# Kernel tuning notes

Measured on AMD Instinct MI355X. Metric: run time of the kernel, lower is better.

The kernel has to match this reference:

```python
import jax, jax.numpy as jnp
import numpy as np

B, S, D = 2, 2048, 1024
N, H = 16, 64  # n_heads, d_head
INIT_STD = 0.02
IGNORE = -100000.0


def setup_inputs() -> dict:
    key = jax.random.key(0)
    ks = jax.random.split(key, 6)
    return {
        "normalized_resid_pre": jax.random.normal(ks[0], (B, S, D), dtype=jnp.float32),
        "W_Q": jax.random.normal(ks[1], (N, D, H), dtype=jnp.float32) * INIT_STD,
        "W_K": jax.random.normal(ks[2], (N, D, H), dtype=jnp.float32) * INIT_STD,
        "W_V": jax.random.normal(ks[3], (N, D, H), dtype=jnp.float32) * INIT_STD,
        "W_O": jax.random.normal(ks[4], (N, H, D), dtype=jnp.float32) * INIT_STD,
        "b_Q": jnp.zeros((N, H), dtype=jnp.float32),
        "b_K": jnp.zeros((N, H), dtype=jnp.float32),
        "b_V": jnp.zeros((N, H), dtype=jnp.float32),
        "b_O": jnp.zeros((D,), dtype=jnp.float32),
    }


def reference(normalized_resid_pre, W_Q, W_K, W_V, W_O, b_Q, b_K, b_V, b_O):
    x = normalized_resid_pre
    q = jnp.einsum('ndh,bpd->bpnh', W_Q, x) + b_Q
    k = jnp.einsum('ndh,bpd->bpnh', W_K, x) + b_K
    v = jnp.einsum('ndh,bpd->bpnh', W_V, x) + b_V
    scores = jnp.einsum('bpnh,bsnh->bnps', q, k) / jnp.sqrt(jnp.float32(H))
    # causal mask: key_pos > query_pos -> IGNORE
    seq = scores.shape[-1]
    mask = jnp.triu(jnp.ones((seq, seq), dtype=bool), k=1)
    scores = jnp.where(mask, jnp.float32(IGNORE), scores)
    attn = jax.nn.softmax(scores, axis=-1)
    z = jnp.einsum('bnps,bsnh->bpnh', attn, v)
    # per-head out-proj then sum over heads
    out = jnp.einsum('bpnh,nhd->bpd', z, W_O) + b_O
    return out
```

## Files before the change

### kernel.cpp

```cpp
#include <hip/hip_runtime.h>
#include <math.h>

#define S_ 2048
#define D_ 1024
#define N_ 16
#define H_ 64
#define M_ 4096

typedef float f4 __attribute__((ext_vector_type(4)));
typedef float f16v __attribute__((ext_vector_type(16)));
typedef short s8v __attribute__((ext_vector_type(8)));
typedef short s4v __attribute__((ext_vector_type(4)));
typedef unsigned short u16;

#define MFMA32(a, b, c) __builtin_amdgcn_mfma_f32_32x32x16_bf16((a), (b), (c), 0, 0, 0)

__device__ __forceinline__ u16 f2bf(float x) {
    unsigned int u = __float_as_uint(x);
    u += 0x7fffu + ((u >> 16) & 1u);
    return (u16)(u >> 16);
}
union FragU { unsigned int u[4]; s4v h[2]; s8v v; };

__device__ __forceinline__ s8v ld8(const u16* p) {
    FragU f;
    f.h[0] = *(const s4v*)(p);
    f.h[1] = *(const s4v*)(p + 4);
    return f.v;
}
__device__ __forceinline__ void st8(u16* p, s8v x) {
    FragU f; f.v = x;
    *(s4v*)(p)     = f.h[0];
    *(s4v*)(p + 4) = f.h[1];
}

__global__ __launch_bounds__(256) void cvt_x(const float* __restrict__ x,
                                             u16* __restrict__ xb)
{
    int i = (blockIdx.x * 256 + threadIdx.x) * 8;
    f4 a = *(const f4*)(x + i);
    f4 b = *(const f4*)(x + i + 4);
    unsigned long long p0 =
        (unsigned long long)f2bf(a[0]) | ((unsigned long long)f2bf(a[1]) << 16) |
        ((unsigned long long)f2bf(a[2]) << 32) | ((unsigned long long)f2bf(a[3]) << 48);
    unsigned long long p1 =
        (unsigned long long)f2bf(b[0]) | ((unsigned long long)f2bf(b[1]) << 16) |
        ((unsigned long long)f2bf(b[2]) << 32) | ((unsigned long long)f2bf(b[3]) << 48);
    *(unsigned long long*)(xb + i)     = p0;
    *(unsigned long long*)(xb + i + 4) = p1;
}

__global__ __launch_bounds__(256) void transW_kernel(
    const float* __restrict__ Wq, const float* __restrict__ Wk, const float* __restrict__ Wv,
    u16* __restrict__ Wc)
{
    const int which = blockIdx.z, n = blockIdx.y, dt = blockIdx.x;
    const float* W = which == 0 ? Wq : (which == 1 ? Wk : Wv);
    __shared__ float t[64][65];
    const int tid = threadIdx.x;
    #pragma unroll
    for (int it = 0; it < 4; ++it) {
        int c = tid + it * 256;
        int d = c >> 4, h4 = c & 15;
        f4 v = *(const f4*)(W + ((size_t)n * 1024 + dt * 64 + d) * 64 + h4 * 4);
        #pragma unroll
        for (int j = 0; j < 4; ++j) t[h4 * 4 + j][d] = v[j];
    }
    __syncthreads();
    #pragma unroll
    for (int it = 0; it < 4; ++it) {
        int c = tid + it * 256;
        int h = c >> 4, d4 = c & 15;
        size_t o = (size_t)(which * 1024 + n * 64 + h) * 1024 + dt * 64 + d4 * 4;
        *(unsigned long long*)(Wc + o) =
            (unsigned long long)f2bf(t[h][d4 * 4 + 0]) |
            ((unsigned long long)f2bf(t[h][d4 * 4 + 1]) << 16) |
            ((unsigned long long)f2bf(t[h][d4 * 4 + 2]) << 32) |
            ((unsigned long long)f2bf(t[h][d4 * 4 + 3]) << 48);
    }
}

__global__ __launch_bounds__(256) void transWo_kernel(
    const float* __restrict__ Wo, u16* __restrict__ WoT)
{
    const int rt = blockIdx.y, ct = blockIdx.x;
    __shared__ float t[64][65];
    const int tid = threadIdx.x;
    #pragma unroll
    for (int it = 0; it < 4; ++it) {
        int c = tid + it * 256;
        int r = c >> 4, c4 = c & 15;
        f4 v = *(const f4*)(Wo + (size_t)(rt * 64 + r) * 1024 + ct * 64 + c4 * 4);
        #pragma unroll
        for (int j = 0; j < 4; ++j) t[c4 * 4 + j][r] = v[j];
    }
    __syncthreads();
    #pragma unroll
    for (int it = 0; it < 4; ++it) {
        int c = tid + it * 256;
        int d = c >> 4, r4 = c & 15;
        size_t o = (size_t)(ct * 64 + d) * 1024 + rt * 64 + r4 * 4;
        *(unsigned long long*)(WoT + o) =
            (unsigned long long)f2bf(t[d][r4 * 4 + 0]) |
            ((unsigned long long)f2bf(t[d][r4 * 4 + 1]) << 16) |
            ((unsigned long long)f2bf(t[d][r4 * 4 + 2]) << 32) |
            ((unsigned long long)f2bf(t[d][r4 * 4 + 3]) << 48);
    }
}

__global__ void bcat_kernel(const float* bq, const float* bk, const float* bv, float* bc)
{
    int i = blockIdx.x * 256 + threadIdx.x;
    bc[i] = i < 1024 ? bq[i] : (i < 2048 ? bk[i - 1024] : bv[i - 2048]);
}

template<int MODE>
__global__ __launch_bounds__(256) void gemm_bf16(
    const u16* __restrict__ A, const u16* __restrict__ B,
    const float* __restrict__ bias,
    u16* __restrict__ outq, u16* __restrict__ outk, u16* __restrict__ outvT,
    float* __restrict__ outf)
{
    __shared__ u16 sm[17408];
    u16* Ash = sm;
    u16* Bsh = sm + 8704;

    const int tid = threadIdx.x;
    const int lane = tid & 63, w = tid >> 6;
    const int wm = w & 1, wn = w >> 1;
    const int l31 = lane & 31, hi = lane >> 5;
    const int m0 = blockIdx.x * 128, n0 = blockIdx.y * 128;

    f16v acc[2][2];
    #pragma unroll
    for (int a = 0; a < 2; ++a)
        #pragma unroll
        for (int b = 0; b < 2; ++b)
            #pragma unroll
            for (int r = 0; r < 16; ++r) acc[a][b][r] = 0.f;

    for (int kt = 0; kt < 16; ++kt) {
        __syncthreads();
        #pragma unroll
        for (int t = 0; t < 4; ++t) {
            int c = tid + t * 256;
            int row = c >> 3, c8 = c & 7;
            int idx = row * 68 + c8 * 8;
            s8v av = *(const s8v*)(A + (size_t)(m0 + row) * 1024 + kt * 64 + c8 * 8);
            s8v bv = *(const s8v*)(B + (size_t)(n0 + row) * 1024 + kt * 64 + c8 * 8);
            st8(&Ash[idx], av);
            st8(&Bsh[idx], bv);
        }
        __syncthreads();
        #pragma unroll
        for (int ks = 0; ks < 4; ++ks) {
            const int off = (2 * ks + hi) * 8;
            s8v af[2], bf[2];
            #pragma unroll
            for (int mb = 0; mb < 2; ++mb)
                af[mb] = ld8(&Ash[(64 * wm + 32 * mb + l31) * 68 + off]);
            #pragma unroll
            for (int nb = 0; nb < 2; ++nb)
                bf[nb] = ld8(&Bsh[(64 * wn + 32 * nb + l31) * 68 + off]);
            #pragma unroll
            for (int mb = 0; mb < 2; ++mb)
                #pragma unroll
                for (int nb = 0; nb < 2; ++nb)
                    acc[mb][nb] = MFMA32(af[mb], bf[nb], acc[mb][nb]);
        }
    }

    __syncthreads();

    if constexpr (MODE == 0) {
        u16* Zw = sm + w * 4096;
        const int which = n0 >> 10;
        #pragma unroll
        for (int nb = 0; nb < 2; ++nb) {
            int nhl = 32 * nb + l31;
            float bv = bias[n0 + 64 * wn + nhl];
            #pragma unroll
            for (int mb = 0; mb < 2; ++mb)
                #pragma unroll
                for (int r = 0; r < 16; ++r) {
                    int ml = 32 * mb + (r & 3) + 8 * (r >> 2) + 4 * hi;
                    u16 hv = f2bf(acc[mb][nb][r] + bv);
                    int idx = (which == 2)
                        ? nhl * 64 + (ml ^ ((nhl & 7) << 3))
                        : ml * 64 + (nhl ^ ((ml & 7) << 3));
                    Zw[idx] = hv;
                }
        }
        __syncthreads();
        const int gmb = m0 + 64 * wm;
        const int gnb = n0 + 64 * wn;
        #pragma unroll
        for (int it = 0; it < 8; ++it) {
            int c = lane + it * 64;
            int row = c >> 3, c8 = c & 7;
            int idx = row * 64 + 8 * (c8 ^ (row & 7));
            s8v val = *(const s8v*)&Zw[idx];
            if (which == 0)
                *(s8v*)(outq + (size_t)(gmb + row) * 1024 + gnb + c8 * 8) = val;
            else if (which == 1)
                *(s8v*)(outk + (size_t)(gmb + row) * 1024 + (gnb - 1024) + c8 * 8) = val;
            else
                *(s8v*)(outvT + (size_t)(gnb - 2048 + row) * 4096 + gmb + c8 * 8) = val;
        }
    } else {
        #pragma unroll
        for (int nb = 0; nb < 2; ++nb) {
            int gcol = n0 + 64 * wn + 32 * nb + l31;
            float bv = bias[gcol];
            #pragma unroll
            for (int mb = 0; mb < 2; ++mb)
                #pragma unroll
                for (int r = 0; r < 16; ++r) {
                    int gm = m0 + 64 * wm + 32 * mb + (r & 3) + 8 * (r >> 2) + 4 * hi;
                    outf[(size_t)gm * 1024 + gcol] = acc[mb][nb][r] + bv;
                }
        }
    }
}

#define SCALE_LOG2 (0.125f * 1.44269504088896340736f)

__global__ __launch_bounds__(256) void attn_mfma(
    const u16* __restrict__ qp, const u16* __restrict__ kp,
    const u16* __restrict__ vTp, u16* __restrict__ zp)
{
    __shared__ u16 sm[8704];
    u16* Ksh = sm;
    u16* Vsh = sm + 4352;

    const int tid = threadIdx.x;
    const int lane = tid & 63, w = tid >> 6;
    const int l31 = lane & 31, hi = lane >> 5;
    const int qt = (int)gridDim.x - 1 - (int)blockIdx.x;
    const int n = blockIdx.y, b = blockIdx.z;
    const int q0 = qt * 128;
    const int qrow = q0 + 32 * w + l31;
    const size_t mrow = (size_t)b * 2048 + qrow;

    s8v qf[4];
    #pragma unroll
    for (int c = 0; c < 4; ++c)
        qf[c] = *(const s8v*)(qp + mrow * 1024 + n * 64 + c * 16 + hi * 8);

    f16v acc[2];
    #pragma unroll
    for (int mb = 0; mb < 2; ++mb)
        #pragma unroll
        for (int r = 0; r < 16; ++r) acc[mb][r] = 0.f;
    float mrun = -1e30f, lrun = 0.f;
    const int nkt = 2 * qt + 2;
    const int wqmax = q0 + 32 * w + 31;

    for (int kt = 0; kt < nkt; ++kt) {
        __syncthreads();
        #pragma unroll
        for (int t2 = 0; t2 < 2; ++t2) {
            int c = tid + t2 * 256;
            int row = c >> 3, c8 = c & 7;
            int idx = row * 68 + c8 * 8;
            s8v kv = *(const s8v*)(kp + ((size_t)b * 2048 + kt * 64 + row) * 1024 + n * 64 + c8 * 8);
            s8v vv = *(const s8v*)(vTp + ((size_t)n * 64 + row) * 4096 + b * 2048 + kt * 64 + c8 * 8);
            st8(&Ksh[idx], kv);
            st8(&Vsh[idx], vv);
        }
        __syncthreads();
        if (64 * kt > wqmax) continue;

        f16v sf[2];
        #pragma unroll
        for (int t = 0; t < 2; ++t) {
            #pragma unroll
            for (int r = 0; r < 16; ++r) sf[t][r] = 0.f;
            int row = 32 * t + l31;
            #pragma unroll
            for (int c = 0; c < 4; ++c) {
                s8v kf = ld8(&Ksh[row * 68 + (2 * c + hi) * 8]);
                sf[t] = MFMA32(kf, qf[c], sf[t]);
            }
        }

        float mloc = -1e30f;
        #pragma unroll
        for (int t = 0; t < 2; ++t)
            #pragma unroll
            for (int r = 0; r < 16; ++r) {
                float sc = sf[t][r] * SCALE_LOG2;
                int sg = kt * 64 + 32 * t + (r & 3) + 8 * (r >> 2) + 4 * hi;
                if (sg > qrow) sc = -1e30f;
                sf[t][r] = sc;
                mloc = fmaxf(mloc, sc);
            }
        mloc = fmaxf(mloc, __shfl_xor(mloc, 32, 64));
        float mnew = fmaxf(mrun, mloc);
        float alpha = exp2f(mrun - mnew);
        float ls = 0.f;
        #pragma unroll
        for (int t = 0; t < 2; ++t)
            #pragma unroll
            for (int r = 0; r < 16; ++r) {
                float pv = exp2f(sf[t][r] - mnew);
                sf[t][r] = pv;
                ls += pv;
            }
        ls += __shfl_xor(ls, 32, 64);
        lrun = lrun * alpha + ls;
        mrun = mnew;
        #pragma unroll
        for (int mb = 0; mb < 2; ++mb)
            #pragma unroll
            for (int r = 0; r < 16; ++r) acc[mb][r] *= alpha;

        s8v pf[4];
        #pragma unroll
        for (int c = 0; c < 4; ++c) {
            const int i0 = 2 * c, i1 = 2 * c + 1;
            const int t0 = i0 >> 2, u0 = i0 & 3;
            const int t1 = i1 >> 2, u1 = i1 & 3;
            unsigned int f00 = (unsigned int)f2bf(sf[t0][4 * u0 + 0]) |
                               ((unsigned int)f2bf(sf[t0][4 * u0 + 1]) << 16);
            unsigned int f01 = (unsigned int)f2bf(sf[t0][4 * u0 + 2]) |
                               ((unsigned int)f2bf(sf[t0][4 * u0 + 3]) << 16);
            unsigned int f10 = (unsigned int)f2bf(sf[t1][4 * u1 + 0]) |
                               ((unsigned int)f2bf(sf[t1][4 * u1 + 1]) << 16);
            unsigned int f11 = (unsigned int)f2bf(sf[t1][4 * u1 + 2]) |
                               ((unsigned int)f2bf(sf[t1][4 * u1 + 3]) << 16);
            unsigned int s0 = hi ? f00 : f10, s1 = hi ? f01 : f11;
            unsigned int r0 = __shfl_xor(s0, 32, 64);
            unsigned int r1 = __shfl_xor(s1, 32, 64);
            FragU f;
            f.u[0] = hi ? r0 : f00;  f.u[1] = hi ? r1 : f01;
            f.u[2] = hi ? f10 : r0;  f.u[3] = hi ? f11 : r1;
            pf[c] = f.v;
        }

        #pragma unroll
        for (int mb = 0; mb < 2; ++mb) {
            int row = 32 * mb + l31;
            #pragma unroll
            for (int c = 0; c < 4; ++c) {
                s8v vf = ld8(&Vsh[row * 68 + (2 * c + hi) * 8]);
                acc[mb] = MFMA32(vf, pf[c], acc[mb]);
            }
        }
    }

    __syncthreads();
    float linv = 1.0f / lrun;
    u16* Z = sm + w * 2048;
    #pragma unroll
    for (int mb = 0; mb < 2; ++mb)
        #pragma unroll
        for (int r = 0; r < 16; ++r) {
            int hcol = 32 * mb + (r & 3) + 8 * (r >> 2) + 4 * hi;
            int idx = l31 * 64 + (hcol ^ ((l31 & 7) << 3));
            Z[idx] = f2bf(acc[mb][r] * linv);
        }
    __syncthreads();
    #pragma unroll
    for (int it = 0; it < 4; ++it) {
        int c = lane + it * 64;
        int row = c >> 3, c8 = c & 7;
        int idx = row * 64 + 8 * (c8 ^ (row & 7));
        *(s8v*)(zp + ((size_t)b * 2048 + q0 + 32 * w + row) * 1024 + n * 64 + c8 * 8) =
            *(const s8v*)&Z[idx];
    }
}

extern "C" void kernel_launch(void* const* d_in, const int* in_sizes, int n_in,
                              void* d_out, int out_size, void* d_ws, size_t ws_size,
                              hipStream_t stream) {
    const float* x  = (const float*)d_in[0];
    const float* Wq = (const float*)d_in[1];
    const float* Wk = (const float*)d_in[2];
    const float* Wv = (const float*)d_in[3];
    const float* Wo = (const float*)d_in[4];
    const float* bq = (const float*)d_in[5];
    const float* bk = (const float*)d_in[6];
    const float* bv = (const float*)d_in[7];
    const float* bO = (const float*)d_in[8];
    float* out = (float*)d_out;

    char* p = (char*)d_ws;
    size_t o = 0;
    auto alloc = [&](size_t bytes) { char* r = p + o; o += bytes; return r; };
    const size_t MB8 = (size_t)M_ * D_ * 2;
    u16* xb   = (u16*)alloc(MB8);
    u16* Wc   = (u16*)alloc((size_t)3072 * 1024 * 2);
    u16* WoT  = (u16*)alloc((size_t)1024 * 1024 * 2);
    float* bc = (float*)alloc(65536);
    u16* qb   = (u16*)alloc(MB8);
    u16* kb   = (u16*)alloc(MB8);
    u16* vTb  = (u16*)alloc(MB8);
    if (ws_size < o) return;
    u16* zb = xb;

    cvt_x<<<2048, 256, 0, stream>>>(x, xb);
    transW_kernel<<<dim3(16, 16, 3), 256, 0, stream>>>(Wq, Wk, Wv, Wc);
    transWo_kernel<<<dim3(16, 16), 256, 0, stream>>>(Wo, WoT);
    bcat_kernel<<<12, 256, 0, stream>>>(bq, bk, bv, bc);
    gemm_bf16<0><<<dim3(32, 24), 256, 0, stream>>>(
        xb, Wc, bc, qb, kb, vTb, nullptr);
    attn_mfma<<<dim3(16, 16, 2), 256, 0, stream>>>(qb, kb, vTb, zb);
    gemm_bf16<1><<<dim3(32, 8), 256, 0, stream>>>(
        zb, WoT, bO, nullptr, nullptr, nullptr, out);
}
```

Baseline: 255.7 us.

## Double-buffer attention K/V via direct global-to-LDS loads with swizzled layout

Replaces the register-staged LDS fills in both the projection GEMM and the attention kernel with global_load_lds 16-byte direct copies, using an XOR-swizzled unpadded LDS layout. Attention now double-buffers K/V tiles so the next tile's load overlaps the current tile's compute. It also folds the softmax scale into Q at projection time, uses packed bf16 conversion instructions, skips the causal mask on fully visible tiles, and defers the running-max rescale when the max grows by at most 8. These aim to cut load latency, bank conflicts and VALU work, but they double attention LDS usage and rely on careful barrier placement for the async loads.

```diff
diff --git a/kernel.cpp b/kernel.cpp
--- a/kernel.cpp
+++ b/kernel.cpp
@@ -3,36 +3,33 @@
 
 #define S_ 2048
 #define D_ 1024
-#define N_ 16
-#define H_ 64
 #define M_ 4096
 
 typedef float f4 __attribute__((ext_vector_type(4)));
 typedef float f16v __attribute__((ext_vector_type(16)));
 typedef short s8v __attribute__((ext_vector_type(8)));
-typedef short s4v __attribute__((ext_vector_type(4)));
 typedef unsigned short u16;
 
-#define MFMA32(a, b, c) __builtin_amdgcn_mfma_f32_32x32x16_bf16((a), (b), (c), 0, 0, 0)
+#define MFMA32(a,b,c) __builtin_amdgcn_mfma_f32_32x32x16_bf16((a),(b),(c),0,0,0)
+#define QSCALE 0.1803368801111204f
+#define NINF  -1e30f
 
 __device__ __forceinline__ u16 f2bf(float x) {
     unsigned int u = __float_as_uint(x);
     u += 0x7fffu + ((u >> 16) & 1u);
     return (u16)(u >> 16);
 }
-union FragU { unsigned int u[4]; s4v h[2]; s8v v; };
-
-__device__ __forceinline__ s8v ld8(const u16* p) {
-    FragU f;
-    f.h[0] = *(const s4v*)(p);
-    f.h[1] = *(const s4v*)(p + 4);
-    return f.v;
-}
-__device__ __forceinline__ void st8(u16* p, s8v x) {
-    FragU f; f.v = x;
-    *(s4v*)(p)     = f.h[0];
-    *(s4v*)(p + 4) = f.h[1];
-}
+__device__ __forceinline__ unsigned int cvtpk(float lo, float hi) {
+    unsigned int r;
+    asm("v_cvt_pk_bf16_f32 %0, %1, %2" : "=v"(r) : "v"(lo), "v"(hi));
+    return r;
+}
+__device__ __forceinline__ void gload16(const void* g, void* l) {
+    __builtin_amdgcn_global_load_lds(
+        (const __attribute__((address_space(1))) unsigned int*)g,
+        (__attribute__((address_space(3))) unsigned int*)l, 16, 0, 0);
+}
+union FragU { unsigned int u[4]; s8v v; };
 
 __global__ __launch_bounds__(256) void cvt_x(const float* __restrict__ x,
                                              u16* __restrict__ xb)
@@ -121,15 +118,18 @@
     u16* __restrict__ outq, u16* __restrict__ outk, u16* __restrict__ outvT,
     float* __restrict__ outf)
 {
-    __shared__ u16 sm[17408];
+    __shared__ u16 sm[16384];
     u16* Ash = sm;
-    u16* Bsh = sm + 8704;
+    u16* Bsh = sm + 8192;
 
     const int tid = threadIdx.x;
     const int lane = tid & 63, w = tid >> 6;
     const int wm = w & 1, wn = w >> 1;
     const int l31 = lane & 31, hi = lane >> 5;
     const int m0 = blockIdx.x * 128, n0 = blockIdx.y * 128;
+    const int srow = lane >> 3;
+    const int sc8 = (lane & 7) ^ srow;
+    const int rx = l31 & 7;
 
     f16v acc[2][2];
     #pragma unroll
@@ -142,26 +142,24 @@
     for (int kt = 0; kt < 16; ++kt) {
         __syncthreads();
         #pragma unroll
-        for (int t = 0; t < 4; ++t) {
-            int c = tid + t * 256;
-            int row = c >> 3, c8 = c & 7;
-            int idx = row * 68 + c8 * 8;
-            s8v av = *(const s8v*)(A + (size_t)(m0 + row) * 1024 + kt * 64 + c8 * 8);
-            s8v bv = *(const s8v*)(B + (size_t)(n0 + row) * 1024 + kt * 64 + c8 * 8);
-            st8(&Ash[idx], av);
-            st8(&Bsh[idx], bv);
+        for (int i = 0; i < 4; ++i) {
+            const int rb = (i * 4 + w) * 8;
+            const int row = rb + srow;
+            gload16(A + (size_t)(m0 + row) * 1024 + kt * 64 + sc8 * 8, Ash + rb * 64);
+            gload16(B + (size_t)(n0 + row) * 1024 + kt * 64 + sc8 * 8, Bsh + rb * 64);
         }
         __syncthreads();
         #pragma unroll
         for (int ks = 0; ks < 4; ++ks) {
-            const int off = (2 * ks + hi) * 8;
             s8v af[2], bf[2];
             #pragma unroll
             for (int mb = 0; mb < 2; ++mb)
-                af[mb] = ld8(&Ash[(64 * wm + 32 * mb + l31) * 68 + off]);
+                af[mb] = *(const s8v*)&Ash[(64 * wm + 32 * mb + l31) * 64 +
+                                           ((2 * ks + hi) ^ rx) * 8];
             #pragma unroll
             for (int nb = 0; nb < 2; ++nb)
-                bf[nb] = ld8(&Bsh[(64 * wn + 32 * nb + l31) * 68 + off]);
+                bf[nb] = *(const s8v*)&Bsh[(64 * wn + 32 * nb + l31) * 64 +
+                                           ((2 * ks + hi) ^ rx) * 8];
             #pragma unroll
             for (int mb = 0; mb < 2; ++mb)
                 #pragma unroll
@@ -184,7 +182,9 @@
                 #pragma unroll
                 for (int r = 0; r < 16; ++r) {
                     int ml = 32 * mb + (r & 3) + 8 * (r >> 2) + 4 * hi;
-                    u16 hv = f2bf(acc[mb][nb][r] + bv);
+                    float vv = acc[mb][nb][r] + bv;
+                    if (which == 0) vv *= QSCALE;
+                    u16 hv = f2bf(vv);
                     int idx = (which == 2)
                         ? nhl * 64 + (ml ^ ((nhl & 7) << 3))
                         : ml * 64 + (nhl ^ ((ml & 7) << 3));
@@ -223,16 +223,11 @@
     }
 }
 
-#define SCALE_LOG2 (0.125f * 1.44269504088896340736f)
-
 __global__ __launch_bounds__(256) void attn_mfma(
     const u16* __restrict__ qp, const u16* __restrict__ kp,
     const u16* __restrict__ vTp, u16* __restrict__ zp)
 {
-    __shared__ u16 sm[8704];
-    u16* Ksh = sm;
-    u16* Vsh = sm + 4352;
-
+    __shared__ u16 sm[16384];
     const int tid = threadIdx.x;
     const int lane = tid & 63, w = tid >> 6;
     const int l31 = lane & 31, hi = lane >> 5;
@@ -240,7 +235,11 @@
     const int n = blockIdx.y, b = blockIdx.z;
     const int q0 = qt * 128;
     const int qrow = q0 + 32 * w + l31;
+    const int wqmin = q0 + 32 * w, wqmax = wqmin + 31;
     const size_t mrow = (size_t)b * 2048 + qrow;
+    const int srow = lane >> 3;
+    const int sc8 = (lane & 7) ^ srow;
+    const int rx = l31 & 7;
 
     s8v qf[4];
     #pragma unroll
@@ -252,101 +251,130 @@
     for (int mb = 0; mb < 2; ++mb)
         #pragma unroll
         for (int r = 0; r < 16; ++r) acc[mb][r] = 0.f;
-    float mrun = -1e30f, lrun = 0.f;
+    float mrun = NINF, lrun = 0.f;
     const int nkt = 2 * qt + 2;
-    const int wqmax = q0 + 32 * w + 31;
-
+
+    auto STAGE = [&](int kt, int bufi) {
+        u16* Kd = sm + bufi * 8192;
+        u16* Vd = Kd + 4096;
+        #pragma unroll
+        for (int i = 0; i < 2; ++i) {
+            const int rb = (i * 4 + w) * 8;
+            const int row = rb + srow;
+            gload16(kp + ((size_t)b * 2048 + kt * 64 + row) * 1024 + n * 64 + sc8 * 8,
+                    Kd + rb * 64);
+            gload16(vTp + ((size_t)n * 64 + row) * 4096 + b * 2048 + kt * 64 + sc8 * 8,
+                    Vd + rb * 64);
+        }
+    };
+
+    STAGE(0, 0);
+    int cur = 0;
     for (int kt = 0; kt < nkt; ++kt) {
         __syncthreads();
-        #pragma unroll
-        for (int t2 = 0; t2 < 2; ++t2) {
-            int c = tid + t2 * 256;
-            int row = c >> 3, c8 = c & 7;
-            int idx = row * 68 + c8 * 8;
-            s8v kv = *(const s8v*)(kp + ((size_t)b * 2048 + kt * 64 + row) * 1024 + n * 64 + c8 * 8);
-            s8v vv = *(const s8v*)(vTp + ((size_t)n * 64 + row) * 4096 + b * 2048 + kt * 64 + c8 * 8);
-            st8(&Ksh[idx], kv);
-            st8(&Vsh[idx], vv);
-        }
-        __syncthreads();
-        if (64 * kt > wqmax) continue;
-
-        f16v sf[2];
-        #pragma unroll
-        for (int t = 0; t < 2; ++t) {
-            #pragma unroll
-            for (int r = 0; r < 16; ++r) sf[t][r] = 0.f;
-            int row = 32 * t + l31;
+        if (kt + 1 < nkt) STAGE(kt + 1, cur ^ 1);
+        if (64 * kt <= wqmax) {
+            const u16* Kd = sm + cur * 8192;
+            const u16* Vd = Kd + 4096;
+
+            f16v sf[2];
+            #pragma unroll
+            for (int t = 0; t < 2; ++t) {
+                #pragma unroll
+                for (int r = 0; r < 16; ++r) sf[t][r] = 0.f;
+                const int row = 32 * t + l31;
+                #pragma unroll
+                for (int c = 0; c < 4; ++c) {
+                    s8v kf = *(const s8v*)&Kd[row * 64 + ((2 * c + hi) ^ rx) * 8];
+                    sf[t] = MFMA32(kf, qf[c], sf[t]);
+                }
+            }
+
+            if (64 * kt + 63 > wqmin) {
+                #pragma unroll
+                for (int t = 0; t < 2; ++t)
+                    #pragma unroll
+                    for (int r = 0; r < 16; ++r) {
+                        const int sg = kt * 64 + 32 * t + (r & 3) + 8 * (r >> 2) + 4 * hi;
+                        if (sg > qrow) sf[t][r] = NINF;
+                    }
+            }
+
+            float ma = NINF, mb2 = NINF, mc = NINF, md = NINF;
+            #pragma unroll
+            for (int t = 0; t < 2; ++t)
+                #pragma unroll
+                for (int r = 0; r < 16; r += 4) {
+                    ma  = fmaxf(ma,  sf[t][r]);
+                    mb2 = fmaxf(mb2, sf[t][r + 1]);
+                    mc  = fmaxf(mc,  sf[t][r + 2]);
+                    md  = fmaxf(md,  sf[t][r + 3]);
+                }
+            float mloc = fmaxf(fmaxf(ma, mb2), fmaxf(mc, md));
+            mloc = fmaxf(mloc, __shfl_xor(mloc, 32, 64));
+
+            float mbase;
+            bool defer = (mloc - mrun <= 8.0f);
+            if (__all(defer)) {
+                mbase = mrun;
+            } else {
+                float mnew = fmaxf(mrun, mloc);
+                float alpha = exp2f(mrun - mnew);
+                lrun *= alpha;
+                #pragma unroll
+                for (int mb = 0; mb < 2; ++mb)
+                    #pragma unroll
+                    for (int r = 0; r < 16; ++r) acc[mb][r] *= alpha;
+                mrun = mnew;
+                mbase = mnew;
+            }
+            float sa = 0.f, sb = 0.f, sc2 = 0.f, sd = 0.f;
+            #pragma unroll
+            for (int t = 0; t < 2; ++t)
+                #pragma unroll
+                for (int r = 0; r < 16; r += 4) {
+                    float p0 = exp2f(sf[t][r]     - mbase);
+                    float p1 = exp2f(sf[t][r + 1] - mbase);
+                    float p2 = exp2f(sf[t][r + 2] - mbase);
+                    float p3 = exp2f(sf[t][r + 3] - mbase);
+                    sf[t][r] = p0; sf[t][r + 1] = p1;
+                    sf[t][r + 2] = p2; sf[t][r + 3] = p3;
+                    sa += p0; sb += p1; sc2 += p2; sd += p3;
+                }
+            float ls = (sa + sb) + (sc2 + sd);
+            ls += __shfl_xor(ls, 32, 64);
+            lrun += ls;
+
+            s8v pf[4];
             #pragma unroll
             for (int c = 0; c < 4; ++c) {
-                s8v kf = ld8(&Ksh[row * 68 + (2 * c + hi) * 8]);
-                sf[t] = MFMA32(kf, qf[c], sf[t]);
+                const int i0 = 2 * c, i1 = 2 * c + 1;
+                const int t0 = i0 >> 2, u0 = i0 & 3;
+                const int t1 = i1 >> 2, u1 = i1 & 3;
+                unsigned int f00 = cvtpk(sf[t0][4 * u0 + 0], sf[t0][4 * u0 + 1]);
+                unsigned int f01 = cvtpk(sf[t0][4 * u0 + 2], sf[t0][4 * u0 + 3]);
+                unsigned int f10 = cvtpk(sf[t1][4 * u1 + 0], sf[t1][4 * u1 + 1]);
+                unsigned int f11 = cvtpk(sf[t1][4 * u1 + 2], sf[t1][4 * u1 + 3]);
+                unsigned int s0 = hi ? f00 : f10, s1 = hi ? f01 : f11;
+                unsigned int r0 = __shfl_xor(s0, 32, 64);
+                unsigned int r1 = __shfl_xor(s1, 32, 64);
+                FragU f;
+                f.u[0] = hi ? r0 : f00;  f.u[1] = hi ? r1 : f01;
+                f.u[2] = hi ? f10 : r0;  f.u[3] = hi ? f11 : r1;
+                pf[c] = f.v;
             }
-        }
-
-        float mloc = -1e30f;
-        #pragma unroll
-        for (int t = 0; t < 2; ++t)
-            #pragma unroll
-            for (int r = 0; r < 16; ++r) {
-                float sc = sf[t][r] * SCALE_LOG2;
-                int sg = kt * 64 + 32 * t + (r & 3) + 8 * (r >> 2) + 4 * hi;
-                if (sg > qrow) sc = -1e30f;
-                sf[t][r] = sc;
-                mloc = fmaxf(mloc, sc);
+
+            #pragma unroll
+            for (int mb = 0; mb < 2; ++mb) {
+                const int row = 32 * mb + l31;
+                #pragma unroll
+                for (int c = 0; c < 4; ++c) {
+                    s8v vf = *(const s8v*)&Vd[row * 64 + ((2 * c + hi) ^ rx) * 8];
+                    acc[mb] = MFMA32(vf, pf[c], acc[mb]);
+                }
             }
-        mloc = fmaxf(mloc, __shfl_xor(mloc, 32, 64));
-        float mnew = fmaxf(mrun, mloc);
-        float alpha = exp2f(mrun - mnew);
-        float ls = 0.f;
-        #pragma unroll
-        for (int t = 0; t < 2; ++t)
-            #pragma unroll
-            for (int r = 0; r < 16; ++r) {
-                float pv = exp2f(sf[t][r] - mnew);
-                sf[t][r] = pv;
-                ls += pv;
-            }
-        ls += __shfl_xor(ls, 32, 64);
-        lrun = lrun * alpha + ls;
-        mrun = mnew;
-        #pragma unroll
-        for (int mb = 0; mb < 2; ++mb)
-            #pragma unroll
-            for (int r = 0; r < 16; ++r) acc[mb][r] *= alpha;
-
-        s8v pf[4];
-        #pragma unroll
-        for (int c = 0; c < 4; ++c) {
-            const int i0 = 2 * c, i1 = 2 * c + 1;
-            const int t0 = i0 >> 2, u0 = i0 & 3;
-            const int t1 = i1 >> 2, u1 = i1 & 3;
-            unsigned int f00 = (unsigned int)f2bf(sf[t0][4 * u0 + 0]) |
-                               ((unsigned int)f2bf(sf[t0][4 * u0 + 1]) << 16);
-            unsigned int f01 = (unsigned int)f2bf(sf[t0][4 * u0 + 2]) |
-                               ((unsigned int)f2bf(sf[t0][4 * u0 + 3]) << 16);
-            unsigned int f10 = (unsigned int)f2bf(sf[t1][4 * u1 + 0]) |
-                               ((unsigned int)f2bf(sf[t1][4 * u1 + 1]) << 16);
-            unsigned int f11 = (unsigned int)f2bf(sf[t1][4 * u1 + 2]) |
-                               ((unsigned int)f2bf(sf[t1][4 * u1 + 3]) << 16);
-            unsigned int s0 = hi ? f00 : f10, s1 = hi ? f01 : f11;
-            unsigned int r0 = __shfl_xor(s0, 32, 64);
-            unsigned int r1 = __shfl_xor(s1, 32, 64);
-            FragU f;
-            f.u[0] = hi ? r0 : f00;  f.u[1] = hi ? r1 : f01;
-            f.u[2] = hi ? f10 : r0;  f.u[3] = hi ? f11 : r1;
-            pf[c] = f.v;
-        }
-
-        #pragma unroll
-        for (int mb = 0; mb < 2; ++mb) {
-            int row = 32 * mb + l31;
-            #pragma unroll
-            for (int c = 0; c < 4; ++c) {
-                s8v vf = ld8(&Vsh[row * 68 + (2 * c + hi) * 8]);
-                acc[mb] = MFMA32(vf, pf[c], acc[mb]);
-            }
-        }
+        }
+        cur ^= 1;
     }
 
     __syncthreads();
```

Measured after the change: 231.2 us. -9.6%, faster.
